# Performance work log

Hardware: AMD Instinct MI355X
Metric: run time of the kernel (lower is better)

Reference implementation:

```python
import jax, jax.numpy as jnp
import numpy as np

EMBED = 1024
HEADS = 16
HEAD_DIM = EMBED // HEADS


def setup_inputs() -> dict:
    key = jax.random.key(0)
    ks = jax.random.split(key, 5)
    s = 0.02
    x = jax.random.normal(ks[0], (2, 2048, EMBED), dtype=jnp.float32)
    W_qkv = jax.random.normal(ks[1], (EMBED, 3 * EMBED), dtype=jnp.float32) * s
    b_qkv = jnp.zeros((3 * EMBED,), dtype=jnp.float32)
    W_proj = jax.random.normal(ks[2], (EMBED, EMBED), dtype=jnp.float32) * s
    b_proj = jnp.zeros((EMBED,), dtype=jnp.float32)
    return {"x": x, "W_qkv": W_qkv, "b_qkv": b_qkv, "W_proj": W_proj, "b_proj": b_proj}


def reference(x, W_qkv, b_qkv, W_proj, b_proj):
    B, N, _ = x.shape
    scale = HEAD_DIM ** -0.5
    qkv = x @ W_qkv + b_qkv                     # [B,N,3E]
    qkv = qkv.reshape(B, N, 3, HEADS, HEAD_DIM)
    q = qkv[:, :, 0].transpose(0, 2, 1, 3) * scale  # [B,H,N,D]
    k = qkv[:, :, 1].transpose(0, 2, 1, 3)
    v = qkv[:, :, 2].transpose(0, 2, 1, 3)
    attn = jnp.einsum('bhnd,bhmd->bhnm', q, k)  # [B,H,N,N]
    attn = jax.nn.softmax(attn, axis=-1)
    out = jnp.einsum('bhnm,bhmd->bhnd', attn, v)  # [B,H,N,D]
    out = out.transpose(0, 2, 1, 3).reshape(B, N, HEADS * HEAD_DIM)
    return out @ W_proj + b_proj
```

## Files before the change

kernel.cpp:

```cpp
#include <hip/hip_runtime.h>
#include <hip/hip_bf16.h>
#include <stdint.h>

typedef unsigned short u16;
typedef __bf16 bf16x8 __attribute__((ext_vector_type(8)));
typedef float f32x4 __attribute__((ext_vector_type(4)));
typedef float f32x16 __attribute__((ext_vector_type(16)));

__device__ __forceinline__ u16 f2bf(float f) {
    union { float f; unsigned u; } x; x.f = f;
    unsigned u = x.u;
    u += 0x7FFFu + ((u >> 16) & 1u);
    return (u16)(u >> 16);
}
__device__ __forceinline__ float bf2f(u16 h) {
    union { unsigned u; float f; } x; x.u = ((unsigned)h) << 16; return x.f;
}

typedef __attribute__((address_space(1))) void gvoid;
typedef __attribute__((address_space(3))) void lvoid;
__device__ __forceinline__ void gl2lds16(const void* g, void* l) {
    __builtin_amdgcn_global_load_lds((gvoid*)g, (lvoid*)l, 16, 0, 0);
}

__global__ __launch_bounds__(256) void prep_kernel(
    const float* __restrict__ x, u16* __restrict__ xb,
    const float* __restrict__ Wqkv, u16* __restrict__ wqkvT,
    const float* __restrict__ Wproj, u16* __restrict__ wprojT)
{
    __shared__ u16 tile[64][65];
    const int blk = blockIdx.x;
    const int tid = threadIdx.x;

    if (blk < 2048) {
        const size_t i = ((size_t)blk * 256 + tid) * 8;
        float4 a = *(const float4*)(x + i);
        float4 b = *(const float4*)(x + i + 4);
        ushort4 oa, ob;
        oa.x = f2bf(a.x); oa.y = f2bf(a.y); oa.z = f2bf(a.z); oa.w = f2bf(a.w);
        ob.x = f2bf(b.x); ob.y = f2bf(b.y); ob.z = f2bf(b.z); ob.w = f2bf(b.w);
        *(ushort4*)(xb + i) = oa;
        *(ushort4*)(xb + i + 4) = ob;
        return;
    }
    const float* in; u16* out; int rows, cols, bx, by;
    if (blk < 2816) { int t = blk - 2048; in = Wqkv;  out = wqkvT;  rows = 1024; cols = 3072; bx = t % 48; by = t / 48; }
    else            { int t = blk - 2816; in = Wproj; out = wprojT; rows = 1024; cols = 1024; bx = t % 16; by = t / 16; }
#pragma unroll
    for (int i = 0; i < 16; i++) {
        int e = i * 256 + tid;
        int r = e >> 6, c = e & 63;
        tile[r][c] = f2bf(in[(size_t)(by * 64 + r) * cols + bx * 64 + c]);
    }
    __syncthreads();
#pragma unroll
    for (int i = 0; i < 16; i++) {
        int e = i * 256 + tid;
        int r = e >> 6, c = e & 63;
        out[(size_t)(bx * 64 + r) * rows + by * 64 + c] = tile[c][r];
    }
}

__global__ __launch_bounds__(256) void gemm_qkv(
    const u16* __restrict__ A, const u16* __restrict__ Bt,
    const float* __restrict__ bias,
    u16* __restrict__ q, u16* __restrict__ ko, u16* __restrict__ vt)
{
    constexpr int K = 1024;
    __shared__ __align__(16) u16 smem[128 * 132];
    u16* sA = smem;
    u16* sB = smem + 8192;
    const int tid = threadIdx.x;
    const int wave = tid >> 6, lane = tid & 63;
    const int quad = lane >> 4, l16 = lane & 15;
    const int wm = (wave >> 1) * 64, wn = (wave & 1) * 64;
    const int m0 = blockIdx.y * 128, n0 = blockIdx.x * 128;
    const int srow = lane >> 3;
    const int scolz = ((lane & 7) ^ srow) * 8;

    f32x4 acc[4][4];
#pragma unroll
    for (int i = 0; i < 4; i++)
#pragma unroll
        for (int j = 0; j < 4; j++)
#pragma unroll
            for (int r = 0; r < 4; r++) acc[i][j][r] = 0.f;

    for (int kt = 0; kt < K; kt += 64) {
        __syncthreads();
#pragma unroll
        for (int t = 0; t < 4; t++) {
            int rb = wave * 32 + t * 8;
            gl2lds16(A  + (size_t)(m0 + rb + srow) * K + kt + scolz, &sA[rb * 64]);
            gl2lds16(Bt + (size_t)(n0 + rb + srow) * K + kt + scolz, &sB[rb * 64]);
        }
        __syncthreads();
#pragma unroll
        for (int kk = 0; kk < 64; kk += 32) {
            bf16x8 af[4], bfr[4];
#pragma unroll
            for (int t = 0; t < 4; t++) {
                int sl = (((kk >> 3) + quad) ^ (l16 & 7)) * 8;
                af[t]  = *(const bf16x8*)&sA[(wm + t * 16 + l16) * 64 + sl];
                bfr[t] = *(const bf16x8*)&sB[(wn + t * 16 + l16) * 64 + sl];
            }
#pragma unroll
            for (int i = 0; i < 4; i++)
#pragma unroll
                for (int j = 0; j < 4; j++)
                    acc[i][j] = __builtin_amdgcn_mfma_f32_16x16x32_bf16(
                        af[i], bfr[j], acc[i][j], 0, 0, 0);
        }
    }

    const float QSCALE = 0.18033688011112042f;
    const float sc = (n0 < 1024) ? QSCALE : 1.0f;
    __syncthreads();
#pragma unroll
    for (int i = 0; i < 4; i++) {
#pragma unroll
        for (int j = 0; j < 4; j++) {
            float bv = bias[n0 + wn + j * 16 + l16];
#pragma unroll
            for (int r = 0; r < 4; r++) {
                float v = (acc[i][j][r] + bv) * sc;
                smem[(wm + i * 16 + quad * 4 + r) * 132 + wn + j * 16 + l16] = f2bf(v);
            }
        }
    }
    __syncthreads();

    if (n0 < 2048) {
        u16* dst = (n0 < 1024) ? q : ko;
#pragma unroll
        for (int it = 0; it < 8; it++) {
            int c = it * 256 + tid;
            int m_l = c >> 4;
            int n8 = (c & 15) * 8;
            uint4 w = *(const uint4*)&smem[m_l * 132 + n8];
            int n = n0 + n8;
            int h = (n & 1023) >> 6, d = n & 63;
            int m = m0 + m_l;
            int b = m >> 11, t = m & 2047;
            *(uint4*)(dst + ((size_t)(b * 16 + h) * 2048 + t) * 64 + d) = w;
        }
    } else {
        int nv = n0 - 2048;
        int n_l = tid & 127, mh = tid >> 7;
        int hh = (nv >> 6) + (n_l >> 6);
        int d = n_l & 63;
        int bb = m0 >> 11, t0 = m0 & 2047;
        u16* vrow = vt + ((size_t)(bb * 16 + hh) * 64 + d) * 2048 + t0 + mh * 64;
#pragma unroll
        for (int it = 0; it < 8; it++) {
            int tch = mh * 64 + it * 8;
            union { u16 s[8]; uint4 w; } pk;
#pragma unroll
            for (int i = 0; i < 8; i++)
                pk.s[i] = smem[(tch + i) * 132 + n_l];
            *(uint4*)(vrow + it * 8) = pk.w;
        }
    }
}

__global__ __launch_bounds__(256, 4) void attn_kernel(
    const u16* __restrict__ q, const u16* __restrict__ ko,
    const u16* __restrict__ vt,
    u16* __restrict__ op0, u16* __restrict__ op1,
    float* __restrict__ lp0, float* __restrict__ lp1)
{
    __shared__ __align__(16) u16 sK[2][64 * 72];
    __shared__ __align__(16) u16 sV[2][64 * 72];

    const int tid = threadIdx.x;
    const int wave = tid >> 6, lane = tid & 63;
    const int l31 = lane & 31, hi = lane >> 5;

    const int lid = blockIdx.x;
    const int xcd = lid & 7, idx = lid >> 3;
    const int h = xcd * 2 + (idx & 1);
    const int b = (idx >> 1) & 1;
    const int q0 = ((idx >> 2) & 15) * 128;
    const int khalf = idx >> 6;
    const int kbase = khalf * 1024;
    const size_t bh = (size_t)(b * 16 + h);

    const u16* qp  = q  + bh * 2048 * 64;
    const u16* kp  = ko + bh * 2048 * 64;
    const u16* vtp = vt + bh * 64 * 2048;

    bf16x8 qf[4];
    {
        const u16* qrow = qp + (size_t)(q0 + wave * 32 + l31) * 64 + hi * 8;
#pragma unroll
        for (int d = 0; d < 4; d++)
            qf[d] = *(const bf16x8*)(qrow + d * 16);
    }

    const int sr0 = tid >> 3;
    const int sc0 = (tid & 7) * 8;
    const int sr1 = sr0 + 32;

    uint4 pk0 = *(const uint4*)(kp + (size_t)(kbase + sr0) * 64 + sc0);
    uint4 pk1 = *(const uint4*)(kp + (size_t)(kbase + sr1) * 64 + sc0);
    uint4 pv0 = *(const uint4*)(vtp + (size_t)sr0 * 2048 + kbase + sc0);
    uint4 pv1 = *(const uint4*)(vtp + (size_t)sr1 * 2048 + kbase + sc0);

    f32x16 accO[2];
#pragma unroll
    for (int d = 0; d < 2; d++)
#pragma unroll
        for (int r = 0; r < 16; r++) accO[d][r] = 0.f;
    float ls[4] = {0.f, 0.f, 0.f, 0.f};

    for (int t = 0; t < 16; ++t) {
        const int cur = t & 1;
        u16* sKc = &sK[cur][0];
        u16* sVc = &sV[cur][0];
        *(uint4*)&sKc[sr0 * 72 + sc0] = pk0;
        *(uint4*)&sKc[sr1 * 72 + sc0] = pk1;
        *(uint4*)&sVc[sr0 * 72 + sc0] = pv0;
        *(uint4*)&sVc[sr1 * 72 + sc0] = pv1;
        if (t < 15) {
            int nt = kbase + (t + 1) * 64;
            pk0 = *(const uint4*)(kp + (size_t)(nt + sr0) * 64 + sc0);
            pk1 = *(const uint4*)(kp + (size_t)(nt + sr1) * 64 + sc0);
            pv0 = *(const uint4*)(vtp + (size_t)sr0 * 2048 + nt + sc0);
            pv1 = *(const uint4*)(vtp + (size_t)sr1 * 2048 + nt + sc0);
        }
        __syncthreads();

#pragma unroll
        for (int rb = 0; rb < 2; rb++) {
            f32x16 S;
#pragma unroll
            for (int r = 0; r < 16; r++) S[r] = 0.f;
            const u16* krd = &sKc[(rb * 32 + l31) * 72 + hi * 8];
#pragma unroll
            for (int d = 0; d < 4; d++) {
                bf16x8 kf = *(const bf16x8*)(krd + d * 16);
                S = __builtin_amdgcn_mfma_f32_32x32x16_bf16(kf, qf[d], S, 0, 0, 0);
            }
            union { float f; unsigned u; } e[16];
#pragma unroll
            for (int r = 0; r < 16; r++) {
                e[r].f = __builtin_amdgcn_exp2f(S[r]);
                ls[r & 3] += e[r].f;
            }
#pragma unroll
            for (int ks2 = 0; ks2 < 2; ks2++) {
                union { unsigned u[4]; bf16x8 v; } pa;
#pragma unroll
                for (int s = 0; s < 4; s++) {
                    unsigned r0 = e[ks2 * 8 + 2 * s].u + 0x8000u;
                    unsigned r1 = e[ks2 * 8 + 2 * s + 1].u + 0x8000u;
                    pa.u[s] = (r1 & 0xFFFF0000u) | (r0 >> 16);
                }
                const int nb = rb * 32 + ks2 * 16 + 4 * hi;
#pragma unroll
                for (int db = 0; db < 2; db++) {
                    const u16* vr = &sVc[(db * 32 + l31) * 72 + nb];
                    union { uint2 w[2]; bf16x8 v; } vf;
                    vf.w[0] = *(const uint2*)(vr);
                    vf.w[1] = *(const uint2*)(vr + 8);
                    accO[db] = __builtin_amdgcn_mfma_f32_32x32x16_bf16(pa.v, vf.v, accO[db], 0, 0, 0);
                }
            }
        }
    }

    u16* op = khalf ? op1 : op0;
    float* lp = khalf ? lp1 : lp0;

    float lsum = (ls[0] + ls[1]) + (ls[2] + ls[3]);
    float ltot = lsum + __shfl_xor(lsum, 32, 64);
    int qq0 = q0 + wave * 32;
    if (hi == 0) lp[bh * 2048 + qq0 + l31] = ltot;

#pragma unroll
    for (int db = 0; db < 2; db++)
#pragma unroll
        for (int r = 0; r < 16; r++) {
            int tq = qq0 + (r & 3) + 8 * (r >> 2) + 4 * hi;
            size_t row = (size_t)b * 2048 + tq;
            op[row * 1024 + h * 64 + db * 32 + l31] = f2bf(accO[db][r]);
        }
}

__global__ __launch_bounds__(256) void combine_kernel(
    const u16* __restrict__ op0, const u16* __restrict__ op1,
    const float* __restrict__ lp0, const float* __restrict__ lp1,
    u16* __restrict__ ob)
{
    const size_t i = ((size_t)blockIdx.x * 256 + threadIdx.x) * 8;
    int m = (int)(i >> 10), e = (int)(i & 1023);
    int b = m >> 11, t = m & 2047, h = e >> 6;
    float inv = 1.f / (lp0[(size_t)(b * 16 + h) * 2048 + t] +
                       lp1[(size_t)(b * 16 + h) * 2048 + t]);
    union { uint4 w; u16 s[8]; } a, c, o;
    a.w = *(const uint4*)(op0 + i);
    c.w = *(const uint4*)(op1 + i);
#pragma unroll
    for (int k = 0; k < 8; k++)
        o.s[k] = f2bf((bf2f(a.s[k]) + bf2f(c.s[k])) * inv);
    *(uint4*)(ob + i) = o.w;
}

__global__ __launch_bounds__(256) void gemm_proj(
    const u16* __restrict__ A, const u16* __restrict__ Bt,
    const float* __restrict__ bias, float* __restrict__ out)
{
    constexpr int K = 1024;
    __shared__ __align__(16) u16 sA[64 * 64];
    __shared__ __align__(16) u16 sB[128 * 64];
    const int tid = threadIdx.x;
    const int wave = tid >> 6, lane = tid & 63;
    const int quad = lane >> 4, l16 = lane & 15;
    const int wm = (wave & 1) * 32, wn = (wave >> 1) * 64;

    const int lid = blockIdx.x;
    const int xcd = lid & 7, idx = lid >> 3;
    const int m0 = (xcd * 8 + (idx & 7)) * 64;
    const int n0 = (idx >> 3) * 128;

    const int srow = lane >> 3;
    const int scolz = ((lane & 7) ^ srow) * 8;

    f32x4 acc[2][4];
#pragma unroll
    for (int i = 0; i < 2; i++)
#pragma unroll
        for (int j = 0; j < 4; j++)
#pragma unroll
            for (int r = 0; r < 4; r++) acc[i][j][r] = 0.f;

    for (int kt = 0; kt < K; kt += 64) {
        __syncthreads();
#pragma unroll
        for (int t = 0; t < 2; t++) {
            int rb = wave * 16 + t * 8;
            gl2lds16(A + (size_t)(m0 + rb + srow) * K + kt + scolz, &sA[rb * 64]);
        }
#pragma unroll
        for (int t = 0; t < 4; t++) {
            int rb = wave * 32 + t * 8;
            gl2lds16(Bt + (size_t)(n0 + rb + srow) * K + kt + scolz, &sB[rb * 64]);
        }
        __syncthreads();
#pragma unroll
        for (int kk = 0; kk < 64; kk += 32) {
            bf16x8 af[2], bfr[4];
            int sl = (((kk >> 3) + quad) ^ (l16 & 7)) * 8;
#pragma unroll
            for (int t = 0; t < 2; t++)
                af[t] = *(const bf16x8*)&sA[(wm + t * 16 + l16) * 64 + sl];
#pragma unroll
            for (int t = 0; t < 4; t++)
                bfr[t] = *(const bf16x8*)&sB[(wn + t * 16 + l16) * 64 + sl];
#pragma unroll
            for (int i = 0; i < 2; i++)
#pragma unroll
                for (int j = 0; j < 4; j++)
                    acc[i][j] = __builtin_amdgcn_mfma_f32_16x16x32_bf16(
                        af[i], bfr[j], acc[i][j], 0, 0, 0);
        }
    }

#pragma unroll
    for (int i = 0; i < 2; i++) {
#pragma unroll
        for (int j = 0; j < 4; j++) {
            int n = n0 + wn + j * 16 + l16;
            float bv = bias[n];
#pragma unroll
            for (int r = 0; r < 4; r++) {
                int m = m0 + wm + i * 16 + quad * 4 + r;
                out[(size_t)m * 1024 + n] = acc[i][j][r] + bv;
            }
        }
    }
}

extern "C" void kernel_launch(void* const* d_in, const int* in_sizes, int n_in,
                              void* d_out, int out_size, void* d_ws, size_t ws_size,
                              hipStream_t stream) {
    const float* x     = (const float*)d_in[0];
    const float* Wqkv  = (const float*)d_in[1];
    const float* bqkv  = (const float*)d_in[2];
    const float* Wproj = (const float*)d_in[3];
    const float* bproj = (const float*)d_in[4];
    float* out = (float*)d_out;
    char* ws = (char*)d_ws;

    u16* wqkvT  = (u16*)(ws);
    u16* wprojT = (u16*)(ws +  6291456);
    u16* xb     = (u16*)(ws +  8388608);
    u16* qb     = (u16*)(ws + 16777216);
    u16* kb     = (u16*)(ws + 25165824);
    u16* vtb    = (u16*)(ws + 33554432);
    u16* ob     = (u16*)(ws + 41943040);

    u16*   op0 = ob;
    u16*   op1 = xb;
    float* lp0 = (float*)wqkvT;
    float* lp1 = (float*)(ws + 262144);

    prep_kernel<<<dim3(3072), 256, 0, stream>>>(x, xb, Wqkv, wqkvT, Wproj, wprojT);
    gemm_qkv<<<dim3(24, 32), 256, 0, stream>>>(xb, wqkvT, bqkv, qb, kb, vtb);
    attn_kernel<<<dim3(1024), 256, 0, stream>>>(qb, kb, vtb, op0, op1, lp0, lp1);
    combine_kernel<<<dim3(2048), 256, 0, stream>>>(op0, op1, lp0, lp1, ob);
    gemm_proj<<<dim3(512), 256, 0, stream>>>(ob, wprojT, bproj, out);
}
```

Baseline: 187.4 us.

## Deepen attention K/V prefetch to two tiles and halve QKV GEMM M-tile

The attention kernel now keeps two register sets of K/V tiles in flight and alternates between the two LDS buffers. This puts global loads two tiles ahead of compute, to hide more memory latency, at the cost of extra registers that may lower occupancy. Separately, the QKV GEMM tile shrinks from 128x128 to 64x128, doubling the grid, with launch bounds requesting 6 blocks per SM. The aim is better CU fill and occupancy, but each block gets less reuse of the B operand.

Measured after the change: 237.3 us. +26.6%, slower.

```diff
diff --git a/kernel.cpp b/kernel.cpp
--- a/kernel.cpp
+++ b/kernel.cpp
@@ -61,26 +61,26 @@
     }
 }
 
-__global__ __launch_bounds__(256) void gemm_qkv(
+__global__ __launch_bounds__(256, 6) void gemm_qkv(
     const u16* __restrict__ A, const u16* __restrict__ Bt,
     const float* __restrict__ bias,
     u16* __restrict__ q, u16* __restrict__ ko, u16* __restrict__ vt)
 {
     constexpr int K = 1024;
-    __shared__ __align__(16) u16 smem[128 * 132];
+    __shared__ __align__(16) u16 smem[64 * 64 + 128 * 64];
     u16* sA = smem;
-    u16* sB = smem + 8192;
+    u16* sB = smem + 4096;
     const int tid = threadIdx.x;
     const int wave = tid >> 6, lane = tid & 63;
     const int quad = lane >> 4, l16 = lane & 15;
-    const int wm = (wave >> 1) * 64, wn = (wave & 1) * 64;
-    const int m0 = blockIdx.y * 128, n0 = blockIdx.x * 128;
+    const int wm = (wave >> 1) * 32, wn = (wave & 1) * 64;
+    const int m0 = blockIdx.y * 64, n0 = blockIdx.x * 128;
     const int srow = lane >> 3;
     const int scolz = ((lane & 7) ^ srow) * 8;
 
-    f32x4 acc[4][4];
-#pragma unroll
-    for (int i = 0; i < 4; i++)
+    f32x4 acc[2][4];
+#pragma unroll
+    for (int i = 0; i < 2; i++)
 #pragma unroll
         for (int j = 0; j < 4; j++)
 #pragma unroll
@@ -88,24 +88,29 @@
 
     for (int kt = 0; kt < K; kt += 64) {
         __syncthreads();
+#pragma unroll
+        for (int t = 0; t < 2; t++) {
+            int rb = wave * 16 + t * 8;
+            gl2lds16(A + (size_t)(m0 + rb + srow) * K + kt + scolz, &sA[rb * 64]);
+        }
 #pragma unroll
         for (int t = 0; t < 4; t++) {
             int rb = wave * 32 + t * 8;
-            gl2lds16(A  + (size_t)(m0 + rb + srow) * K + kt + scolz, &sA[rb * 64]);
             gl2lds16(Bt + (size_t)(n0 + rb + srow) * K + kt + scolz, &sB[rb * 64]);
         }
         __syncthreads();
 #pragma unroll
         for (int kk = 0; kk < 64; kk += 32) {
-            bf16x8 af[4], bfr[4];
-#pragma unroll
-            for (int t = 0; t < 4; t++) {
-                int sl = (((kk >> 3) + quad) ^ (l16 & 7)) * 8;
-                af[t]  = *(const bf16x8*)&sA[(wm + t * 16 + l16) * 64 + sl];
+            bf16x8 af[2], bfr[4];
+            int sl = (((kk >> 3) + quad) ^ (l16 & 7)) * 8;
+#pragma unroll
+            for (int t = 0; t < 2; t++)
+                af[t] = *(const bf16x8*)&sA[(wm + t * 16 + l16) * 64 + sl];
+#pragma unroll
+            for (int t = 0; t < 4; t++)
                 bfr[t] = *(const bf16x8*)&sB[(wn + t * 16 + l16) * 64 + sl];
-            }
-#pragma unroll
-            for (int i = 0; i < 4; i++)
+#pragma unroll
+            for (int i = 0; i < 2; i++)
 #pragma unroll
                 for (int j = 0; j < 4; j++)
                     acc[i][j] = __builtin_amdgcn_mfma_f32_16x16x32_bf16(
@@ -117,7 +122,7 @@
     const float sc = (n0 < 1024) ? QSCALE : 1.0f;
     __syncthreads();
 #pragma unroll
-    for (int i = 0; i < 4; i++) {
+    for (int i = 0; i < 2; i++) {
 #pragma unroll
         for (int j = 0; j < 4; j++) {
             float bv = bias[n0 + wn + j * 16 + l16];
@@ -133,7 +138,7 @@
     if (n0 < 2048) {
         u16* dst = (n0 < 1024) ? q : ko;
 #pragma unroll
-        for (int it = 0; it < 8; it++) {
+        for (int it = 0; it < 4; it++) {
             int c = it * 256 + tid;
             int m_l = c >> 4;
             int n8 = (c & 15) * 8;
@@ -150,10 +155,10 @@
         int hh = (nv >> 6) + (n_l >> 6);
         int d = n_l & 63;
         int bb = m0 >> 11, t0 = m0 & 2047;
-        u16* vrow = vt + ((size_t)(bb * 16 + hh) * 64 + d) * 2048 + t0 + mh * 64;
-#pragma unroll
-        for (int it = 0; it < 8; it++) {
-            int tch = mh * 64 + it * 8;
+        u16* vrow = vt + ((size_t)(bb * 16 + hh) * 64 + d) * 2048 + t0 + mh * 32;
+#pragma unroll
+        for (int it = 0; it < 4; it++) {
+            int tch = mh * 32 + it * 8;
             union { u16 s[8]; uint4 w; } pk;
 #pragma unroll
             for (int i = 0; i < 8; i++)
@@ -201,10 +206,14 @@
     const int sc0 = (tid & 7) * 8;
     const int sr1 = sr0 + 32;
 
-    uint4 pk0 = *(const uint4*)(kp + (size_t)(kbase + sr0) * 64 + sc0);
-    uint4 pk1 = *(const uint4*)(kp + (size_t)(kbase + sr1) * 64 + sc0);
-    uint4 pv0 = *(const uint4*)(vtp + (size_t)sr0 * 2048 + kbase + sc0);
-    uint4 pv1 = *(const uint4*)(vtp + (size_t)sr1 * 2048 + kbase + sc0);
+    uint4 ak0 = *(const uint4*)(kp + (size_t)(kbase + sr0) * 64 + sc0);
+    uint4 ak1 = *(const uint4*)(kp + (size_t)(kbase + sr1) * 64 + sc0);
+    uint4 av0 = *(const uint4*)(vtp + (size_t)sr0 * 2048 + kbase + sc0);
+    uint4 av1 = *(const uint4*)(vtp + (size_t)sr1 * 2048 + kbase + sc0);
+    uint4 bk0 = *(const uint4*)(kp + (size_t)(kbase + 64 + sr0) * 64 + sc0);
+    uint4 bk1 = *(const uint4*)(kp + (size_t)(kbase + 64 + sr1) * 64 + sc0);
+    uint4 bv0 = *(const uint4*)(vtp + (size_t)sr0 * 2048 + kbase + 64 + sc0);
+    uint4 bv1 = *(const uint4*)(vtp + (size_t)sr1 * 2048 + kbase + 64 + sc0);
 
     f32x16 accO[2];
 #pragma unroll
@@ -213,23 +222,7 @@
         for (int r = 0; r < 16; r++) accO[d][r] = 0.f;
     float ls[4] = {0.f, 0.f, 0.f, 0.f};
 
-    for (int t = 0; t < 16; ++t) {
-        const int cur = t & 1;
-        u16* sKc = &sK[cur][0];
-        u16* sVc = &sV[cur][0];
-        *(uint4*)&sKc[sr0 * 72 + sc0] = pk0;
-        *(uint4*)&sKc[sr1 * 72 + sc0] = pk1;
-        *(uint4*)&sVc[sr0 * 72 + sc0] = pv0;
-        *(uint4*)&sVc[sr1 * 72 + sc0] = pv1;
-        if (t < 15) {
-            int nt = kbase + (t + 1) * 64;
-            pk0 = *(const uint4*)(kp + (size_t)(nt + sr0) * 64 + sc0);
-            pk1 = *(const uint4*)(kp + (size_t)(nt + sr1) * 64 + sc0);
-            pv0 = *(const uint4*)(vtp + (size_t)sr0 * 2048 + nt + sc0);
-            pv1 = *(const uint4*)(vtp + (size_t)sr1 * 2048 + nt + sc0);
-        }
-        __syncthreads();
-
+    auto compute = [&](const u16* sKc, const u16* sVc) {
 #pragma unroll
         for (int rb = 0; rb < 2; rb++) {
             f32x16 S;
@@ -267,6 +260,36 @@
                 }
             }
         }
+    };
+
+    for (int t2 = 0; t2 < 8; ++t2) {
+        const int tA = t2 * 2;
+        *(uint4*)&sK[0][sr0 * 72 + sc0] = ak0;
+        *(uint4*)&sK[0][sr1 * 72 + sc0] = ak1;
+        *(uint4*)&sV[0][sr0 * 72 + sc0] = av0;
+        *(uint4*)&sV[0][sr1 * 72 + sc0] = av1;
+        __syncthreads();
+        if (tA + 2 < 16) {
+            int nt = kbase + (tA + 2) * 64;
+            ak0 = *(const uint4*)(kp + (size_t)(nt + sr0) * 64 + sc0);
+            ak1 = *(const uint4*)(kp + (size_t)(nt + sr1) * 64 + sc0);
+            av0 = *(const uint4*)(vtp + (size_t)sr0 * 2048 + nt + sc0);
+            av1 = *(const uint4*)(vtp + (size_t)sr1 * 2048 + nt + sc0);
+        }
+        compute(&sK[0][0], &sV[0][0]);
+        *(uint4*)&sK[1][sr0 * 72 + sc0] = bk0;
+        *(uint4*)&sK[1][sr1 * 72 + sc0] = bk1;
+        *(uint4*)&sV[1][sr0 * 72 + sc0] = bv0;
+        *(uint4*)&sV[1][sr1 * 72 + sc0] = bv1;
+        __syncthreads();
+        if (tA + 3 < 16) {
+            int nt = kbase + (tA + 3) * 64;
+            bk0 = *(const uint4*)(kp + (size_t)(nt + sr0) * 64 + sc0);
+            bk1 = *(const uint4*)(kp + (size_t)(nt + sr1) * 64 + sc0);
+            bv0 = *(const uint4*)(vtp + (size_t)sr0 * 2048 + nt + sc0);
+            bv1 = *(const uint4*)(vtp + (size_t)sr1 * 2048 + nt + sc0);
+        }
+        compute(&sK[1][0], &sV[1][0]);
     }
 
     u16* op = khalf ? op1 : op0;
@@ -406,7 +429,7 @@
     float* lp1 = (float*)(ws + 262144);
 
     prep_kernel<<<dim3(3072), 256, 0, stream>>>(x, xb, Wqkv, wqkvT, Wproj, wprojT);
-    gemm_qkv<<<dim3(24, 32), 256, 0, stream>>>(xb, wqkvT, bqkv, qb, kb, vtb);
+    gemm_qkv<<<dim3(24, 64), 256, 0, stream>>>(xb, wqkvT, bqkv, qb, kb, vtb);
     attn_kernel<<<dim3(1024), 256, 0, stream>>>(qb, kb, vtb, op0, op1, lp0, lp1);
     combine_kernel<<<dim3(2048), 256, 0, stream>>>(op0, op1, lp0, lp1, ob);
     gemm_proj<<<dim3(512), 256, 0, stream>>>(ob, wprojT, bproj, out);
```
